# Kernel tuning notes

Hardware: AMD Instinct MI355X
Metric: run time of the kernel (lower is better)

The kernel has to match this reference:

```python
import jax, jax.numpy as jnp
import numpy as np

H = 8        # num_heads
D = 768      # d_model
DH = D // H  # d_head = 96


def setup_inputs() -> dict:
    key = jax.random.key(0)
    ks = jax.random.split(key, 12)
    B, S = 4, 2048
    s_in = 1.0 / np.sqrt(D)
    s_cat = 1.0 / np.sqrt(D)
    return {
        "input_querys": jax.random.normal(ks[0], (B, S, D), jnp.float32),
        "input_key": jax.random.normal(ks[1], (B, S, D), jnp.float32),
        "input_values": jax.random.normal(ks[2], (B, S, D), jnp.float32),
        # per-head projection weights, stacked over the head axis
        "Wq": jax.random.normal(ks[3], (H, D, DH), jnp.float32) * s_in,
        "bq": jax.random.normal(ks[4], (H, DH), jnp.float32) * s_in,
        "Wk": jax.random.normal(ks[5], (H, D, DH), jnp.float32) * s_in,
        "bk": jax.random.normal(ks[6], (H, DH), jnp.float32) * s_in,
        "Wv": jax.random.normal(ks[7], (H, D, DH), jnp.float32) * s_in,
        "bv": jax.random.normal(ks[8], (H, DH), jnp.float32) * s_in,
        # output linear: (H*DH) -> D
        "Wo": jax.random.normal(ks[9], (H * DH, D), jnp.float32) * s_cat,
        "bo": jax.random.normal(ks[10], (D,), jnp.float32) * s_cat,
    }


def reference(input_querys, input_key, input_values, Wq, bq, Wk, bk, Wv, bv, Wo, bo):
    # Per-head linear projections (vectorized over the head axis)
    # q/k/v: [B,S,D] -> [B,H,S,DH]
    Q = jnp.einsum("bsd,hdk->bhsk", input_querys, Wq) + bq[None, :, None, :]
    K = jnp.einsum("bsd,hdk->bhsk", input_key, Wk) + bk[None, :, None, :]
    V = jnp.einsum("bsd,hdk->bhsk", input_values, Wv) + bv[None, :, None, :]

    scale = 1.0 / jnp.sqrt(jnp.asarray(DH, Q.dtype))
    scores = jnp.einsum("bhsk,bhtk->bhst", Q, K) * scale  # [B,H,S,S]
    attn = jax.nn.softmax(scores, axis=-1)
    out = jnp.einsum("bhst,bhtk->bhsk", attn, V)  # [B,H,S,DH]

    # concat heads (head-major order matches torch.cat over ModuleList)
    B, _, S, _ = out.shape
    cat = out.transpose(0, 2, 1, 3).reshape(B, S, H * DH)
    return cat @ Wo + bo
```

## Files before the change

kernel.cpp:

```cpp
#include <hip/hip_runtime.h>


typedef unsigned short u16;
typedef _Float16 h16;
typedef h16 h16x8 __attribute__((ext_vector_type(8)));
typedef __fp16 fp16x2 __attribute__((ext_vector_type(2)));
typedef __fp16 fp16x4 __attribute__((ext_vector_type(4)));
typedef unsigned short u16x8 __attribute__((ext_vector_type(8)));
typedef unsigned short u16x4 __attribute__((ext_vector_type(4)));
typedef float f32x4 __attribute__((ext_vector_type(4)));

__device__ __forceinline__ u16 f2h(float f) {
  union { h16 h; u16 u; } c; c.h = (h16)f; return c.u;
}

__device__ __forceinline__ void gll16(const void* g, void* l) {
  __builtin_amdgcn_global_load_lds(
      (const __attribute__((address_space(1))) void*)g,
      (__attribute__((address_space(3))) void*)l, 16, 0, 0);
}

__global__ __launch_bounds__(256) void prep_kernel(
    const float* __restrict__ Wq, const float* __restrict__ Wk,
    const float* __restrict__ Wv, const float* __restrict__ Wo,
    const float* __restrict__ Xk, const float* __restrict__ Xv,
    const float* __restrict__ Xq,
    u16* __restrict__ WqT, u16* __restrict__ WkT,
    u16* __restrict__ WvT, u16* __restrict__ WoT,
    u16* __restrict__ Xk16, u16* __restrict__ Xv16, u16* __restrict__ Xq16)
{
  const int bid = blockIdx.x;
  const int tid = threadIdx.x;

  if (bid >= 432) {
    const int i = bid - 432;
    const int t = i / 3072;
    const long e = ((long)(i % 3072) * 256 + tid) * 8;
    const float* src = (t == 0) ? Xk : (t == 1) ? Xv : Xq;
    u16* dst = (t == 0) ? Xk16 : (t == 1) ? Xv16 : Xq16;
    f32x4 a = *(const f32x4*)(&src[e]);
    f32x4 b = *(const f32x4*)(&src[e + 4]);
    u16x8 v;
    #pragma unroll
    for (int j = 0; j < 4; j++) { v[j] = f2h(a[j]); v[4 + j] = f2h(b[j]); }
    *(u16x8*)(&dst[e]) = v;
    return;
  }

  if (bid < 288) {
    __shared__ u16 Lt[96][72];
    const int w = bid / 96;
    const int r = bid % 96;
    const int h = r / 12, dt = r % 12;
    const float* W = (w == 0) ? Wq : (w == 1) ? Wk : Wv;
    u16* T = (w == 0) ? WqT : (w == 1) ? WkT : WvT;
    const float* src = W + (size_t)h * 73728 + (size_t)dt * 64 * 96;
    #pragma unroll
    for (int p = 0; p < 6; p++) {
      const int lin = p * 1024 + tid * 4;
      f32x4 v = *(const f32x4*)(&src[lin]);
      const int d = lin / 96, kk = lin % 96;
      #pragma unroll
      for (int j = 0; j < 4; j++) Lt[kk + j][d] = f2h(v[j]);
    }
    __syncthreads();
    #pragma unroll
    for (int c = 0; c < 3; c++) {
      const int ch = c * 256 + tid;
      const int kk = ch >> 3, dc = ch & 7;
      u16x8 o = *(const u16x8*)(&Lt[kk][dc * 8]);
      *(u16x8*)(&T[(size_t)(h * 96 + kk) * 768 + dt * 64 + dc * 8]) = o;
    }
    return;
  }

  {
    __shared__ u16 Lo[64][72];
    const int i = bid - 288;
    const int kt = i / 12, nt = i % 12;
    const float* src = Wo + (size_t)(kt * 64) * 768 + nt * 64;
    #pragma unroll
    for (int p = 0; p < 4; p++) {
      const int lin = p * 1024 + tid * 4;
      const int kr = lin >> 6, nc = lin & 63;
      f32x4 v = *(const f32x4*)(&src[(size_t)kr * 768 + nc]);
      #pragma unroll
      for (int j = 0; j < 4; j++) Lo[nc + j][kr] = f2h(v[j]);
    }
    __syncthreads();
    #pragma unroll
    for (int c = 0; c < 2; c++) {
      const int ch = c * 256 + tid;
      const int nr = ch >> 3, kc = ch & 7;
      u16x8 o = *(const u16x8*)(&Lo[nr][kc * 8]);
      *(u16x8*)(&WoT[(size_t)(nt * 64 + nr) * 768 + kt * 64 + kc * 8]) = o;
    }
  }
}

#define GK 768

__global__ __launch_bounds__(256) void gemm_qkv(
    const u16* __restrict__ Xq16, const u16* __restrict__ Xk16,
    const u16* __restrict__ Xv16, const u16* __restrict__ WT,
    const float* __restrict__ bq, const float* __restrict__ bk,
    const float* __restrict__ bv,
    u16* __restrict__ Q16, u16* __restrict__ K16, u16* __restrict__ VT)
{
  const int z = blockIdx.z;
  const u16* BT = WT + (size_t)z * 589824;
  const float* bias = (z == 0) ? bq : (z == 1) ? bk : bv;
  const u16* A = (z == 0) ? Xq16 : (z == 1) ? Xk16 : Xv16;

  __shared__ __align__(16) u16 S[16384];
  u16* As = S;
  u16* Bs = S + 8192;

  const int tid = threadIdx.x;
  const int wave = tid >> 6;
  const int lane = tid & 63;
  const int quad = lane >> 4;
  const int l16 = lane & 15;
  const int m0 = blockIdx.x * 128;
  const int n0 = blockIdx.y * 128;

  f32x4 acc[2][8];
  #pragma unroll
  for (int i = 0; i < 2; i++)
    #pragma unroll
    for (int j = 0; j < 8; j++) acc[i][j] = (f32x4){0.f, 0.f, 0.f, 0.f};

  int srow[4], scol[4];
  #pragma unroll
  for (int p = 0; p < 4; p++) {
    const int c = p * 256 + tid;
    srow[p] = c >> 3;
    scol[p] = ((c & 7) ^ (srow[p] & 7)) << 3;
  }
  const int x7 = (l16 & 7) << 3;

  for (int kt = 0; kt < 12; kt++) {
    const int k0 = kt * 64;
    #pragma unroll
    for (int p = 0; p < 4; p++) {
      gll16(&A[(size_t)(m0 + srow[p]) * GK + k0 + scol[p]],
            As + (size_t)(p * 256 + wave * 64) * 8);
      gll16(&BT[(size_t)(n0 + srow[p]) * GK + k0 + scol[p]],
            Bs + (size_t)(p * 256 + wave * 64) * 8);
    }
    __syncthreads();

    #pragma unroll
    for (int ks2 = 0; ks2 < 2; ks2++) {
      const int cc = (ks2 * 32 + quad * 8) ^ x7;
      h16x8 af[2], bf[8];
      #pragma unroll
      for (int mf = 0; mf < 2; mf++)
        af[mf] = *(const h16x8*)(&As[(wave * 32 + mf * 16 + l16) * 64 + cc]);
      #pragma unroll
      for (int nf = 0; nf < 8; nf++)
        bf[nf] = *(const h16x8*)(&Bs[(nf * 16 + l16) * 64 + cc]);
      #pragma unroll
      for (int mf = 0; mf < 2; mf++)
        #pragma unroll
        for (int nf = 0; nf < 8; nf++)
          acc[mf][nf] = __builtin_amdgcn_mfma_f32_16x16x32_f16(af[mf], bf[nf], acc[mf][nf], 0, 0, 0);
    }
    __syncthreads();
  }

  if (z == 2) {
    const int b = m0 >> 11, s0 = m0 & 2047;
    u16* Ts = S;
    #pragma unroll
    for (int half = 0; half < 2; half++) {
      __syncthreads();
      #pragma unroll
      for (int nf2 = 0; nf2 < 4; nf2++) {
        const int nf = half * 4 + nf2;
        const float bv2 = bias[n0 + nf * 16 + l16];
        #pragma unroll
        for (int mf = 0; mf < 2; mf++)
          #pragma unroll
          for (int r = 0; r < 4; r++)
            Ts[(nf2 * 16 + l16) * 136 + wave * 32 + mf * 16 + quad * 4 + r] =
                f2h(acc[mf][nf][r] + bv2);
      }
      __syncthreads();
      #pragma unroll
      for (int p = 0; p < 4; p++) {
        const int c = p * 256 + tid;
        const int row = c >> 4, col8 = (c & 15) * 8;
        u16x8 o8 = *(const u16x8*)(&Ts[row * 136 + col8]);
        *(u16x8*)(&VT[(size_t)b * 768 * 2048 +
                      (size_t)(n0 + half * 64 + row) * 2048 + s0 + col8]) = o8;
      }
    }
    return;
  }

  u16* Yr = (z == 0) ? Q16 : K16;
  #pragma unroll
  for (int nf = 0; nf < 8; nf++) {
    const int n = n0 + nf * 16 + l16;
    const float bv2 = bias[n];
    #pragma unroll
    for (int mf = 0; mf < 2; mf++) {
      const int m = m0 + wave * 32 + mf * 16 + quad * 4;
      #pragma unroll
      for (int r = 0; r < 4; r++)
        Yr[(size_t)(m + r) * GK + n] = f2h(acc[mf][nf][r] + bv2);
    }
  }
}

__global__ __launch_bounds__(256) void gemm_o(
    const u16* __restrict__ A, const u16* __restrict__ BT,
    const float* __restrict__ bias, float* __restrict__ Y)
{
  __shared__ __align__(16) u16 S[16384];
  u16* As = S;
  u16* Bs = S + 8192;

  const int tid = threadIdx.x;
  const int wave = tid >> 6;
  const int lane = tid & 63;
  const int quad = lane >> 4;
  const int l16 = lane & 15;
  const int m0 = blockIdx.x * 128;
  const int n0 = blockIdx.y * 128;

  f32x4 acc[2][8];
  #pragma unroll
  for (int i = 0; i < 2; i++)
    #pragma unroll
    for (int j = 0; j < 8; j++) acc[i][j] = (f32x4){0.f, 0.f, 0.f, 0.f};

  int srow[4], scol[4];
  #pragma unroll
  for (int p = 0; p < 4; p++) {
    const int c = p * 256 + tid;
    srow[p] = c >> 3;
    scol[p] = ((c & 7) ^ (srow[p] & 7)) << 3;
  }
  const int x7 = (l16 & 7) << 3;

  for (int kt = 0; kt < 12; kt++) {
    const int k0 = kt * 64;
    #pragma unroll
    for (int p = 0; p < 4; p++) {
      gll16(&A[(size_t)(m0 + srow[p]) * GK + k0 + scol[p]],
            As + (size_t)(p * 256 + wave * 64) * 8);
      gll16(&BT[(size_t)(n0 + srow[p]) * GK + k0 + scol[p]],
            Bs + (size_t)(p * 256 + wave * 64) * 8);
    }
    __syncthreads();

    #pragma unroll
    for (int ks2 = 0; ks2 < 2; ks2++) {
      const int cc = (ks2 * 32 + quad * 8) ^ x7;
      h16x8 af[2], bf[8];
      #pragma unroll
      for (int mf = 0; mf < 2; mf++)
        af[mf] = *(const h16x8*)(&As[(wave * 32 + mf * 16 + l16) * 64 + cc]);
      #pragma unroll
      for (int nf = 0; nf < 8; nf++)
        bf[nf] = *(const h16x8*)(&Bs[(nf * 16 + l16) * 64 + cc]);
      #pragma unroll
      for (int mf = 0; mf < 2; mf++)
        #pragma unroll
        for (int nf = 0; nf < 8; nf++)
          acc[mf][nf] = __builtin_amdgcn_mfma_f32_16x16x32_f16(af[mf], bf[nf], acc[mf][nf], 0, 0, 0);
    }
    __syncthreads();
  }

  #pragma unroll
  for (int nf = 0; nf < 8; nf++) {
    const int n = n0 + nf * 16 + l16;
    const float bv = bias[n];
    #pragma unroll
    for (int mf = 0; mf < 2; mf++) {
      const int m = m0 + wave * 32 + mf * 16 + quad * 4;
      #pragma unroll
      for (int r = 0; r < 4; r++)
        Y[(size_t)(m + r) * GK + n] = acc[mf][nf][r] + bv;
    }
  }
}

#define SEQ 2048
#define NT 32
#define LQK 104
#define LVT 72
#define LPS 72

__global__ __launch_bounds__(512, 4) void attn_kernel(
    const u16* __restrict__ Q, const u16* __restrict__ K,
    const u16* __restrict__ VT, u16* __restrict__ O)
{
  __shared__ __align__(16) u16 Ks[2][64 * LQK];
  __shared__ __align__(16) u16 Vt[2][96 * LVT];
  __shared__ __align__(16) u16 Ps[8][16 * LPS];

  const int tid = threadIdx.x;
  const int wave = tid >> 6;
  const int lane = tid & 63;
  const int quad = lane >> 4;
  const int l16 = lane & 15;

  const int bh = blockIdx.y;
  const int b = bh >> 3, h = bh & 7;
  const int q0 = blockIdx.x * 128;

  const size_t batch_off = (size_t)b * SEQ * 768;
  const u16* Kg = K + batch_off + h * 96;
  const u16* Vg = VT + (size_t)b * 768 * 2048 + (size_t)(h * 96) * 2048;

  h16x8 qf[3];
  {
    const u16* Qrow = Q + batch_off + (size_t)(q0 + wave * 16 + l16) * 768 + h * 96 + quad * 8;
    #pragma unroll
    for (int ks = 0; ks < 3; ks++) qf[ks] = *(const h16x8*)(&Qrow[ks * 32]);
  }

  const int kr0 = tid / 12, kc0 = (tid % 12) * 8;
  const int kr1 = (tid + 512) / 12, kc1 = ((tid + 512) % 12) * 8;
  const int vr0 = tid >> 3, vc0 = (tid & 7) * 8;
  const int vr1 = (tid + 512) >> 3, vc1 = ((tid + 512) & 7) * 8;
  const bool extra = tid < 256;

  f32x4 o[6];
  #pragma unroll
  for (int i = 0; i < 6; i++) o[i] = (f32x4){0.f, 0.f, 0.f, 0.f};
  float m_raw = -1e30f, lrow = 0.f;
  const float sc = 0.14724498f;

  u16* Pw = &Ps[wave][0];

  u16x8 kA, kB, vA, vB;
  kA = *(const u16x8*)(&Kg[(size_t)kr0 * 768 + kc0]);
  vA = *(const u16x8*)(&Vg[(size_t)vr0 * 2048 + vc0]);
  if (extra) {
    kB = *(const u16x8*)(&Kg[(size_t)kr1 * 768 + kc1]);
    vB = *(const u16x8*)(&Vg[(size_t)vr1 * 2048 + vc1]);
  }
  *(u16x8*)(&Ks[0][kr0 * LQK + kc0]) = kA;
  *(u16x8*)(&Vt[0][vr0 * LVT + vc0]) = vA;
  if (extra) {
    *(u16x8*)(&Ks[0][kr1 * LQK + kc1]) = kB;
    *(u16x8*)(&Vt[0][vr1 * LVT + vc1]) = vB;
  }
  {
    const u16* Kn = Kg + (size_t)64 * 768;
    const u16* Vn = Vg + 64;
    kA = *(const u16x8*)(&Kn[(size_t)kr0 * 768 + kc0]);
    vA = *(const u16x8*)(&Vn[(size_t)vr0 * 2048 + vc0]);
    if (extra) {
      kB = *(const u16x8*)(&Kn[(size_t)kr1 * 768 + kc1]);
      vB = *(const u16x8*)(&Vn[(size_t)vr1 * 2048 + vc1]);
    }
  }
  __syncthreads();

  for (int kt = 0; kt < NT; kt++) {
    const int cur = kt & 1;
    const u16* Kc = &Ks[cur][0];
    const u16* Vc = &Vt[cur][0];

    f32x4 s[4];
    #pragma unroll
    for (int kf = 0; kf < 4; kf++) s[kf] = (f32x4){0.f, 0.f, 0.f, 0.f};
    __builtin_amdgcn_s_setprio(1);
    #pragma unroll
    for (int ks = 0; ks < 3; ks++) {
      #pragma unroll
      for (int kf = 0; kf < 4; kf++) {
        h16x8 a = *(const h16x8*)(&Kc[(kf * 16 + l16) * LQK + ks * 32 + quad * 8]);
        s[kf] = __builtin_amdgcn_mfma_f32_16x16x32_f16(a, qf[ks], s[kf], 0, 0, 0);
      }
    }
    __builtin_amdgcn_s_setprio(0);

    float mx = s[0][0];
    #pragma unroll
    for (int kf = 0; kf < 4; kf++)
      #pragma unroll
      for (int r = 0; r < 4; r++) mx = fmaxf(mx, s[kf][r]);
    mx = fmaxf(mx, __shfl_xor(mx, 16));
    mx = fmaxf(mx, __shfl_xor(mx, 32));
    if (__any(mx > m_raw + 54.0f)) {
      const float mnew = fmaxf(m_raw, mx);
      const float alpha = exp2f(sc * (m_raw - mnew));
      lrow *= alpha;
      #pragma unroll
      for (int nfo = 0; nfo < 6; nfo++)
        #pragma unroll
        for (int r = 0; r < 4; r++) o[nfo][r] *= alpha;
      m_raw = mnew;
    }
    const float c0 = sc * m_raw;
    float ps = 0.f;
    #pragma unroll
    for (int kf = 0; kf < 4; kf++)
      #pragma unroll
      for (int r = 0; r < 4; r++) {
        float p = exp2f(fmaf(s[kf][r], sc, -c0));
        s[kf][r] = p;
        ps += p;
      }
    lrow += ps;

    #pragma unroll
    for (int kf = 0; kf < 4; kf++) {
      fp16x2 a2 = __builtin_amdgcn_cvt_pkrtz(s[kf][0], s[kf][1]);
      fp16x2 b2 = __builtin_amdgcn_cvt_pkrtz(s[kf][2], s[kf][3]);
      fp16x4 w4; w4[0] = a2[0]; w4[1] = a2[1]; w4[2] = b2[0]; w4[3] = b2[1];
      *(fp16x4*)(&Pw[l16 * LPS + kf * 16 + quad * 4]) = w4;
    }

    __builtin_amdgcn_s_setprio(1);
    #pragma unroll
    for (int ks = 0; ks < 2; ks++) {
      h16x8 pfr = *(const h16x8*)(&Pw[l16 * LPS + ks * 32 + quad * 8]);
      #pragma unroll
      for (int nfo = 0; nfo < 6; nfo++) {
        h16x8 vfr = *(const h16x8*)(&Vc[(nfo * 16 + l16) * LVT + ks * 32 + quad * 8]);
        o[nfo] = __builtin_amdgcn_mfma_f32_16x16x32_f16(vfr, pfr, o[nfo], 0, 0, 0);
      }
    }
    __builtin_amdgcn_s_setprio(0);

    if (kt + 1 < NT) {
      u16* Kw = &Ks[cur ^ 1][0];
      u16* Vw = &Vt[cur ^ 1][0];
      *(u16x8*)(&Kw[kr0 * LQK + kc0]) = kA;
      *(u16x8*)(&Vw[vr0 * LVT + vc0]) = vA;
      if (extra) {
        *(u16x8*)(&Kw[kr1 * LQK + kc1]) = kB;
        *(u16x8*)(&Vw[vr1 * LVT + vc1]) = vB;
      }
      if (kt + 2 < NT) {
        const u16* Kn = Kg + (size_t)(kt + 2) * 64 * 768;
        const u16* Vn = Vg + (size_t)(kt + 2) * 64;
        kA = *(const u16x8*)(&Kn[(size_t)kr0 * 768 + kc0]);
        vA = *(const u16x8*)(&Vn[(size_t)vr0 * 2048 + vc0]);
        if (extra) {
          kB = *(const u16x8*)(&Kn[(size_t)kr1 * 768 + kc1]);
          vB = *(const u16x8*)(&Vn[(size_t)vr1 * 2048 + vc1]);
        }
      }
      __syncthreads();
    }
  }

  lrow += __shfl_xor(lrow, 16);
  lrow += __shfl_xor(lrow, 32);
  const float inv = 1.0f / lrow;
  u16* Ob = O + batch_off + (size_t)(q0 + wave * 16 + l16) * 768 + h * 96;
  #pragma unroll
  for (int nfo = 0; nfo < 6; nfo++) {
    fp16x2 lo = __builtin_amdgcn_cvt_pkrtz(o[nfo][0] * inv, o[nfo][1] * inv);
    fp16x2 hi = __builtin_amdgcn_cvt_pkrtz(o[nfo][2] * inv, o[nfo][3] * inv);
    *(fp16x2*)(&Ob[nfo * 16 + quad * 4]) = lo;
    *(fp16x2*)(&Ob[nfo * 16 + quad * 4 + 2]) = hi;
  }
}

extern "C" void kernel_launch(void* const* d_in, const int* in_sizes, int n_in,
                              void* d_out, int out_size, void* d_ws, size_t ws_size,
                              hipStream_t stream) {
  const float* Xq = (const float*)d_in[0];
  const float* Xk = (const float*)d_in[1];
  const float* Xv = (const float*)d_in[2];
  const float* Wq = (const float*)d_in[3];
  const float* bq = (const float*)d_in[4];
  const float* Wk = (const float*)d_in[5];
  const float* bk = (const float*)d_in[6];
  const float* Wv = (const float*)d_in[7];
  const float* bv = (const float*)d_in[8];
  const float* Wo = (const float*)d_in[9];
  const float* bo = (const float*)d_in[10];

  u16* wsu = (u16*)d_ws;
  u16* WT   = wsu;
  u16* WoT  = wsu + 3 * 589824;
  u16* Q16  = wsu + 4 * 589824;
  u16* Xk16 = Q16 + 6291456;
  u16* Xv16 = Xk16 + 6291456;
  u16* Xq16 = Xv16 + 6291456;

  u16* outu = (u16*)d_out;
  u16* VTb = outu;
  u16* K16 = outu + 6291456;

  u16* A16 = Xk16;

  prep_kernel<<<9648, 256, 0, stream>>>(
      Wq, Wk, Wv, Wo, Xk, Xv, Xq,
      WT, WT + 589824, WT + 2 * 589824, WoT, Xk16, Xv16, Xq16);
  gemm_qkv<<<dim3(64, 6, 3), 256, 0, stream>>>(
      Xq16, Xk16, Xv16, WT, bq, bk, bv, Q16, K16, VTb);
  attn_kernel<<<dim3(16, 32), 512, 0, stream>>>(Q16, K16, VTb, A16);
  gemm_o<<<dim3(64, 6), 256, 0, stream>>>(A16, WoT, bo, (float*)d_out);
}
```

Before: 286.7 us.

## Double-buffer GEMM LDS tiles with async prefetch of next K-slice

Rewrites the QKV and output-projection GEMM main loops to use two LDS buffers with K-slices of 32. The next slice is issued with global_load_lds while the current one feeds MFMAs, synchronised by explicit vmcnt waits and barriers. This aims to hide global load latency that the previous load-sync-compute loop exposed. It drops the XOR swizzle, which may add LDS bank conflicts, and doubles the barrier count per K.

```diff
diff --git a/kernel.cpp b/kernel.cpp
--- a/kernel.cpp
+++ b/kernel.cpp
@@ -112,9 +112,7 @@
   const float* bias = (z == 0) ? bq : (z == 1) ? bk : bv;
   const u16* A = (z == 0) ? Xq16 : (z == 1) ? Xk16 : Xv16;
 
-  __shared__ __align__(16) u16 S[16384];
-  u16* As = S;
-  u16* Bs = S + 8192;
+  __shared__ __align__(16) u16 Sb[16384];
 
   const int tid = threadIdx.x;
   const int wave = tid >> 6;
@@ -130,48 +128,57 @@
     #pragma unroll
     for (int j = 0; j < 8; j++) acc[i][j] = (f32x4){0.f, 0.f, 0.f, 0.f};
 
-  int srow[4], scol[4];
-  #pragma unroll
-  for (int p = 0; p < 4; p++) {
-    const int c = p * 256 + tid;
-    srow[p] = c >> 3;
-    scol[p] = ((c & 7) ^ (srow[p] & 7)) << 3;
-  }
-  const int x7 = (l16 & 7) << 3;
-
-  for (int kt = 0; kt < 12; kt++) {
-    const int k0 = kt * 64;
-    #pragma unroll
-    for (int p = 0; p < 4; p++) {
-      gll16(&A[(size_t)(m0 + srow[p]) * GK + k0 + scol[p]],
-            As + (size_t)(p * 256 + wave * 64) * 8);
-      gll16(&BT[(size_t)(n0 + srow[p]) * GK + k0 + scol[p]],
-            Bs + (size_t)(p * 256 + wave * 64) * 8);
-    }
-    __syncthreads();
-
-    #pragma unroll
-    for (int ks2 = 0; ks2 < 2; ks2++) {
-      const int cc = (ks2 * 32 + quad * 8) ^ x7;
-      h16x8 af[2], bf[8];
-      #pragma unroll
-      for (int mf = 0; mf < 2; mf++)
-        af[mf] = *(const h16x8*)(&As[(wave * 32 + mf * 16 + l16) * 64 + cc]);
+  const int c0 = tid, c1 = tid + 256;
+  const u16* gA0 = A + (size_t)(m0 + (c0 >> 2)) * GK + (c0 & 3) * 8;
+  const u16* gA1 = A + (size_t)(m0 + (c1 >> 2)) * GK + (c1 & 3) * 8;
+  const u16* gB0 = BT + (size_t)(n0 + (c0 >> 2)) * GK + (c0 & 3) * 8;
+  const u16* gB1 = BT + (size_t)(n0 + (c1 >> 2)) * GK + (c1 & 3) * 8;
+  const int ld0 = (wave * 64) * 8;
+  const int ld1 = (256 + wave * 64) * 8;
+
+#define STAGE(buf, kt) do {                                        \
+    const int k0_ = (kt) * 32;                                     \
+    u16* dst_ = Sb + (buf) * 8192;                                 \
+    gll16(gA0 + k0_, dst_ + ld0);                                  \
+    gll16(gA1 + k0_, dst_ + ld1);                                  \
+    gll16(gB0 + k0_, dst_ + 4096 + ld0);                           \
+    gll16(gB1 + k0_, dst_ + 4096 + ld1);                           \
+  } while (0)
+
+  STAGE(0, 0);
+  int buf = 0;
+  for (int kt = 0; kt < 24; kt++) {
+    if (kt + 1 < 24) {
+      STAGE(buf ^ 1, kt + 1);
+      asm volatile("s_waitcnt vmcnt(4)" ::: "memory");
+    } else {
+      asm volatile("s_waitcnt vmcnt(0)" ::: "memory");
+    }
+    __builtin_amdgcn_s_barrier();
+
+    const u16* As = Sb + buf * 8192;
+    const u16* Bs = As + 4096;
+    h16x8 af[2], bf[8];
+    #pragma unroll
+    for (int mf = 0; mf < 2; mf++)
+      af[mf] = *(const h16x8*)(&As[(wave * 32 + mf * 16 + l16) * 32 + quad * 8]);
+    #pragma unroll
+    for (int nf = 0; nf < 8; nf++)
+      bf[nf] = *(const h16x8*)(&Bs[(nf * 16 + l16) * 32 + quad * 8]);
+    #pragma unroll
+    for (int mf = 0; mf < 2; mf++)
       #pragma unroll
       for (int nf = 0; nf < 8; nf++)
-        bf[nf] = *(const h16x8*)(&Bs[(nf * 16 + l16) * 64 + cc]);
-      #pragma unroll
-      for (int mf = 0; mf < 2; mf++)
-        #pragma unroll
-        for (int nf = 0; nf < 8; nf++)
-          acc[mf][nf] = __builtin_amdgcn_mfma_f32_16x16x32_f16(af[mf], bf[nf], acc[mf][nf], 0, 0, 0);
-    }
-    __syncthreads();
-  }
+        acc[mf][nf] = __builtin_amdgcn_mfma_f32_16x16x32_f16(af[mf], bf[nf], acc[mf][nf], 0, 0, 0);
+
+    __builtin_amdgcn_s_barrier();
+    buf ^= 1;
+  }
+#undef STAGE
 
   if (z == 2) {
     const int b = m0 >> 11, s0 = m0 & 2047;
-    u16* Ts = S;
+    u16* Ts = Sb;
     #pragma unroll
     for (int half = 0; half < 2; half++) {
       __syncthreads();
@@ -218,9 +225,7 @@
     const u16* __restrict__ A, const u16* __restrict__ BT,
     const float* __restrict__ bias, float* __restrict__ Y)
 {
-  __shared__ __align__(16) u16 S[16384];
-  u16* As = S;
-  u16* Bs = S + 8192;
+  __shared__ __align__(16) u16 Sb[16384];
 
   const int tid = threadIdx.x;
   const int wave = tid >> 6;
@@ -236,44 +241,53 @@
     #pragma unroll
     for (int j = 0; j < 8; j++) acc[i][j] = (f32x4){0.f, 0.f, 0.f, 0.f};
 
-  int srow[4], scol[4];
-  #pragma unroll
-  for (int p = 0; p < 4; p++) {
-    const int c = p * 256 + tid;
-    srow[p] = c >> 3;
-    scol[p] = ((c & 7) ^ (srow[p] & 7)) << 3;
-  }
-  const int x7 = (l16 & 7) << 3;
-
-  for (int kt = 0; kt < 12; kt++) {
-    const int k0 = kt * 64;
-    #pragma unroll
-    for (int p = 0; p < 4; p++) {
-      gll16(&A[(size_t)(m0 + srow[p]) * GK + k0 + scol[p]],
-            As + (size_t)(p * 256 + wave * 64) * 8);
-      gll16(&BT[(size_t)(n0 + srow[p]) * GK + k0 + scol[p]],
-            Bs + (size_t)(p * 256 + wave * 64) * 8);
-    }
-    __syncthreads();
-
-    #pragma unroll
-    for (int ks2 = 0; ks2 < 2; ks2++) {
-      const int cc = (ks2 * 32 + quad * 8) ^ x7;
-      h16x8 af[2], bf[8];
-      #pragma unroll
-      for (int mf = 0; mf < 2; mf++)
-        af[mf] = *(const h16x8*)(&As[(wave * 32 + mf * 16 + l16) * 64 + cc]);
+  const int c0 = tid, c1 = tid + 256;
+  const u16* gA0 = A + (size_t)(m0 + (c0 >> 2)) * GK + (c0 & 3) * 8;
+  const u16* gA1 = A + (size_t)(m0 + (c1 >> 2)) * GK + (c1 & 3) * 8;
+  const u16* gB0 = BT + (size_t)(n0 + (c0 >> 2)) * GK + (c0 & 3) * 8;
+  const u16* gB1 = BT + (size_t)(n0 + (c1 >> 2)) * GK + (c1 & 3) * 8;
+  const int ld0 = (wave * 64) * 8;
+  const int ld1 = (256 + wave * 64) * 8;
+
+#define STAGE(buf, kt) do {                                        \
+    const int k0_ = (kt) * 32;                                     \
+    u16* dst_ = Sb + (buf) * 8192;                                 \
+    gll16(gA0 + k0_, dst_ + ld0);                                  \
+    gll16(gA1 + k0_, dst_ + ld1);                                  \
+    gll16(gB0 + k0_, dst_ + 4096 + ld0);                           \
+    gll16(gB1 + k0_, dst_ + 4096 + ld1);                           \
+  } while (0)
+
+  STAGE(0, 0);
+  int buf = 0;
+  for (int kt = 0; kt < 24; kt++) {
+    if (kt + 1 < 24) {
+      STAGE(buf ^ 1, kt + 1);
+      asm volatile("s_waitcnt vmcnt(4)" ::: "memory");
+    } else {
+      asm volatile("s_waitcnt vmcnt(0)" ::: "memory");
+    }
+    __builtin_amdgcn_s_barrier();
+
+    const u16* As = Sb + buf * 8192;
+    const u16* Bs = As + 4096;
+    h16x8 af[2], bf[8];
+    #pragma unroll
+    for (int mf = 0; mf < 2; mf++)
+      af[mf] = *(const h16x8*)(&As[(wave * 32 + mf * 16 + l16) * 32 + quad * 8]);
+    #pragma unroll
+    for (int nf = 0; nf < 8; nf++)
+      bf[nf] = *(const h16x8*)(&Bs[(nf * 16 + l16) * 32 + quad * 8]);
+    #pragma unroll
+    for (int mf = 0; mf < 2; mf++)
       #pragma unroll
       for (int nf = 0; nf < 8; nf++)
-        bf[nf] = *(const h16x8*)(&Bs[(nf * 16 + l16) * 64 + cc]);
-      #pragma unroll
-      for (int mf = 0; mf < 2; mf++)
-        #pragma unroll
-        for (int nf = 0; nf < 8; nf++)
-          acc[mf][nf] = __builtin_amdgcn_mfma_f32_16x16x32_f16(af[mf], bf[nf], acc[mf][nf], 0, 0, 0);
-    }
-    __syncthreads();
-  }
+        acc[mf][nf] = __builtin_amdgcn_mfma_f32_16x16x32_f16(af[mf], bf[nf], acc[mf][nf], 0, 0, 0);
+
+    __builtin_amdgcn_s_barrier();
+    buf ^= 1;
+  }
+#undef STAGE
 
   #pragma unroll
   for (int nf = 0; nf < 8; nf++) {
@@ -399,13 +413,13 @@
         for (int r = 0; r < 4; r++) o[nfo][r] *= alpha;
       m_raw = mnew;
     }
-    const float c0 = sc * m_raw;
+    const float c0f = sc * m_raw;
     float ps = 0.f;
     #pragma unroll
     for (int kf = 0; kf < 4; kf++)
       #pragma unroll
       for (int r = 0; r < 4; r++) {
-        float p = exp2f(fmaf(s[kf][r], sc, -c0));
+        float p = exp2f(fmaf(s[kf][r], sc, -c0f));
         s[kf][r] = p;
         ps += p;
       }
```

Measured after the change: 286.0 us. About the same (-0.3%).
